# Kernel tuning notes

Measured on AMD Instinct MI355X. Metric: run time of the kernel, lower is better.

Reference implementation:

```python
import jax, jax.numpy as jnp
import numpy as np

SEQ_LEN = 2048
DIM = 1024
HEADS = 16
DIM_HEAD = 64
INNER = HEADS * DIM_HEAD
BASE = 10000.0


def rope_tables(seq_len, head_dim):
    inv_freq = 1.0 / (BASE ** (jnp.arange(0, head_dim, 2, dtype=jnp.float32) / head_dim))
    t = jnp.arange(seq_len, dtype=jnp.float32)
    freqs = jnp.einsum('i,j->ij', t, inv_freq)          # [n, d/2]
    emb = jnp.concatenate([freqs, freqs], axis=-1)       # [n, d]
    return jnp.cos(emb), jnp.sin(emb)                    # each [n, d]


def rotate_half(x):
    d = x.shape[-1] // 2
    return jnp.concatenate([-x[..., d:], x[..., :d]], axis=-1)


def setup_inputs() -> dict:
    key = jax.random.key(0)
    ks = jax.random.split(key, 5)
    x = jax.random.normal(ks[0], (2, SEQ_LEN, DIM), dtype=jnp.float32)
    W_qkv = jax.random.normal(ks[1], (DIM, 3 * INNER), dtype=jnp.float32) * (DIM ** -0.5)
    W_out = jax.random.normal(ks[2], (INNER, DIM), dtype=jnp.float32) * (INNER ** -0.5)
    b_out = jnp.zeros((DIM,), dtype=jnp.float32)
    ln_g = jnp.ones((DIM,), dtype=jnp.float32)
    ln_b = jnp.zeros((DIM,), dtype=jnp.float32)
    return {"x": x, "W_qkv": W_qkv, "W_out": W_out, "b_out": b_out, "ln_g": ln_g, "ln_b": ln_b}


def reference(x, W_qkv, W_out, b_out, ln_g, ln_b):
    b, n, _ = x.shape
    # LayerNorm
    mu = jnp.mean(x, axis=-1, keepdims=True)
    var = jnp.mean(jnp.square(x - mu), axis=-1, keepdims=True)
    xn = (x - mu) * jax.lax.rsqrt(var + 1e-5) * ln_g + ln_b
    # QKV projection -> [b, h, n, d]
    qkv = xn @ W_qkv                                   # [b, n, 3*inner]
    q, k, v = jnp.split(qkv, 3, axis=-1)
    def to_heads(t):
        return t.reshape(b, n, HEADS, DIM_HEAD).transpose(0, 2, 1, 3)
    q, k, v = to_heads(q), to_heads(k), to_heads(v)
    # RoPE
    cos, sin = rope_tables(n, DIM_HEAD)                # [n, d]
    cos = cos[None, None]                              # [1,1,n,d]
    sin = sin[None, None]
    q = q * cos + rotate_half(q) * sin
    k = k * cos + rotate_half(k) * sin
    # Attention
    scale = DIM_HEAD ** -0.5
    dots = jnp.einsum('bhid,bhjd->bhij', q, k) * scale  # [b,h,n,n]
    causal = jnp.tril(jnp.ones((n, n), dtype=bool))
    dots = jnp.where(causal[None, None], dots, jnp.float32(-jnp.inf))
    attn = jax.nn.softmax(dots, axis=-1)
    out = jnp.einsum('bhij,bhjd->bhid', attn, v)       # [b,h,n,d]
    out = out.transpose(0, 2, 1, 3).reshape(b, n, INNER)
    return out @ W_out + b_out
```

## Files before the change

### kernel.cpp

```cpp
#include <hip/hip_runtime.h>
#include <hip/hip_bf16.h>

#define SEQ    2048
#define DMODEL 1024
#define HEADS  16
#define DHEAD  64
#define BATCH  2
#define TOK    (BATCH * SEQ)
#define NQKV   (3 * DMODEL)
#define QK_SCALE (0.125f * 1.4426950408889634f)

typedef __attribute__((ext_vector_type(8))) short bf16x8;
typedef __attribute__((ext_vector_type(4))) float f32x4;

__device__ __forceinline__ float bf2f(ushort u) {
  union { unsigned int i; float f; } v; v.i = ((unsigned int)u) << 16; return v.f;
}
__device__ __forceinline__ ushort f2bf(float f) {
  union { float f; unsigned int i; } v; v.f = f;
  unsigned int r = (v.i + 0x7fffu + ((v.i >> 16) & 1u)) >> 16;
  return (ushort)r;
}

__device__ __forceinline__ int swz(int row, int byteoff) {
  return row * 128 + (byteoff ^ ((row & 7) << 4));
}
__device__ __forceinline__ int kperm(int s) {
  return (s & 0x20) | ((s & 0x0C) << 1) | ((s & 0x10) >> 2) | (s & 3);
}

#define GLL16(g, l)                                                                     \
  __builtin_amdgcn_global_load_lds((const __attribute__((address_space(1))) void*)(g),  \
                                   (__attribute__((address_space(3))) void*)(l), 16, 0, 0)

__global__ __launch_bounds__(256) void ln_kernel(const float* __restrict__ x,
                                                 const float* __restrict__ g,
                                                 const float* __restrict__ b,
                                                 ushort* __restrict__ xn) {
  int t = blockIdx.x;
  int tid = threadIdx.x;
  const float* row = x + (size_t)t * DMODEL;
  float4 v = *(const float4*)(row + tid * 4);
  float s  = v.x + v.y + v.z + v.w;
  float s2 = v.x * v.x + v.y * v.y + v.z * v.z + v.w * v.w;
#pragma unroll
  for (int m = 32; m >= 1; m >>= 1) {
    s  += __shfl_down(s, m);
    s2 += __shfl_down(s2, m);
  }
  __shared__ float ws[4], ws2[4];
  if ((tid & 63) == 0) { ws[tid >> 6] = s; ws2[tid >> 6] = s2; }
  __syncthreads();
  s  = ws[0] + ws[1] + ws[2] + ws[3];
  s2 = ws2[0] + ws2[1] + ws2[2] + ws2[3];
  float mu  = s * (1.f / DMODEL);
  float var = s2 * (1.f / DMODEL) - mu * mu;
  float rs  = rsqrtf(var + 1e-5f);
  float4 gv = *(const float4*)(g + tid * 4);
  float4 bv = *(const float4*)(b + tid * 4);
  ushort4 o;
  o.x = f2bf((v.x - mu) * rs * gv.x + bv.x);
  o.y = f2bf((v.y - mu) * rs * gv.y + bv.y);
  o.z = f2bf((v.z - mu) * rs * gv.z + bv.z);
  o.w = f2bf((v.w - mu) * rs * gv.w + bv.w);
  *(ushort4*)(xn + (size_t)t * DMODEL + tid * 4) = o;
}

__global__ void transpose_f2b(const float* __restrict__ in, ushort* __restrict__ out,
                              int R, int C) {
  __shared__ float tile[32][33];
  int c0 = blockIdx.x * 32, r0 = blockIdx.y * 32;
  int x = threadIdx.x, y = threadIdx.y;
#pragma unroll
  for (int i = 0; i < 32; i += 8) tile[y + i][x] = in[(size_t)(r0 + y + i) * C + c0 + x];
  __syncthreads();
#pragma unroll
  for (int i = 0; i < 32; i += 8) out[(size_t)(c0 + y + i) * R + r0 + x] = f2bf(tile[x][y + i]);
}

__global__ void rope_tab_kernel(float* __restrict__ ct, float* __restrict__ st) {
  int n = blockIdx.x, d = threadIdx.x;
  float invf = expf(-logf(10000.f) * (float)(d & 31) * (1.f / 32.f));
  float a = (float)n * invf;
  ct[n * DHEAD + d] = cosf(a);
  st[n * DHEAD + d] = sinf(a);
}

template<int EPI>
__global__ __launch_bounds__(256) void gemm_bt(const ushort* __restrict__ A,
                                               const ushort* __restrict__ BT,
                                               float* __restrict__ Cf,
                                               const float* __restrict__ bias,
                                               ushort* __restrict__ qh,
                                               ushort* __restrict__ kh,
                                               ushort* __restrict__ vh,
                                               const float* __restrict__ ct,
                                               const float* __restrict__ st,
                                               int M, int N, int K) {
  __shared__ __align__(16) ushort As[128 * 32];
  __shared__ __align__(16) ushort Bs[128 * 32];
  int tid = threadIdx.x;
  int w = tid >> 6, lane = tid & 63;
  int lrow = lane & 15, g = lane >> 4;
  int m0 = blockIdx.y * 128, n0 = blockIdx.x * 128;
  int wr = (w >> 1) * 64, wc = (w & 1) * 64;
  int grow = lane >> 2;
  int gcol = ((lane & 3) ^ ((grow >> 1) & 3)) * 8;
  ushort* ldsA0 = As + w * 512;
  ushort* ldsA1 = As + 2048 + w * 512;
  ushort* ldsB0 = Bs + w * 512;
  ushort* ldsB1 = Bs + 2048 + w * 512;
  int fcol = (g ^ ((lrow >> 1) & 3)) * 8;
  f32x4 acc[4][4] = {};
  for (int k0 = 0; k0 < K; k0 += 32) {
    __syncthreads();
    GLL16(A  + (size_t)(m0 + w * 16 + grow) * K + k0 + gcol, ldsA0);
    GLL16(A  + (size_t)(m0 + 64 + w * 16 + grow) * K + k0 + gcol, ldsA1);
    GLL16(BT + (size_t)(n0 + w * 16 + grow) * K + k0 + gcol, ldsB0);
    GLL16(BT + (size_t)(n0 + 64 + w * 16 + grow) * K + k0 + gcol, ldsB1);
    __syncthreads();
    bf16x8 af[4], bfr[4];
#pragma unroll
    for (int i = 0; i < 4; i++) af[i]  = *(const bf16x8*)(As + (wr + i * 16 + lrow) * 32 + fcol);
#pragma unroll
    for (int i = 0; i < 4; i++) bfr[i] = *(const bf16x8*)(Bs + (wc + i * 16 + lrow) * 32 + fcol);
    __builtin_amdgcn_s_setprio(1);
#pragma unroll
    for (int mf = 0; mf < 4; mf++)
#pragma unroll
      for (int nf = 0; nf < 4; nf++)
        acc[mf][nf] = __builtin_amdgcn_mfma_f32_16x16x32_bf16(af[mf], bfr[nf], acc[mf][nf], 0, 0, 0);
    __builtin_amdgcn_s_setprio(0);
  }
#pragma unroll
  for (int mf = 0; mf < 4; mf++)
#pragma unroll
    for (int nf = 0; nf < 4; nf++) {
      int col = n0 + wc + nf * 16 + lrow;
#pragma unroll
      for (int r = 0; r < 4; r++) {
        int rowi = m0 + wr + mf * 16 + g * 4 + r;
        float val = acc[mf][nf][r];
        if (EPI == 2) {
          Cf[(size_t)rowi * N + col] = val + bias[col];
        } else {
          int mat = col >> 10, c1 = col & 1023;
          int h = c1 >> 6, d = c1 & 63;
          int bb = rowi >> 11, n = rowi & (SEQ - 1);
          if (mat < 2) {
            float partner = acc[mf][nf ^ 2][r];
            float cs = ct[n * DHEAD + d], sn = st[n * DHEAD + d];
            float sgn = (d & 32) ? 1.f : -1.f;
            val = val * cs + sgn * partner * sn;
            if (mat == 0) val *= QK_SCALE;
          }
          ushort* dst = (mat == 0) ? qh : (mat == 1) ? kh : vh;
          dst[((size_t)(bb * HEADS + h) * SEQ + n) * DHEAD + d] = f2bf(val);
        }
      }
    }
}

__global__ __launch_bounds__(256) void attn_kernel(const ushort* __restrict__ q,
                                                   const ushort* __restrict__ k,
                                                   const ushort* __restrict__ v,
                                                   ushort* __restrict__ ao) {
  int wgid = blockIdx.x + gridDim.x * blockIdx.y;
  int xcd = wgid & 7, idx = wgid >> 3;
  int bh = xcd * 4 + (idx & 3);
  int qt = 31 - (idx >> 2);
  int tid = threadIdx.x, w = tid >> 6, lane = tid & 63;
  int lrow = lane & 15, g = lane >> 4;
  __shared__ __align__(16) ushort Ks[2][64 * 64];
  __shared__ __align__(16) ushort Vt[2][64 * 64];
  const ushort* qb = q + (size_t)bh * SEQ * DHEAD;
  const ushort* kb = k + (size_t)bh * SEQ * DHEAD;
  const ushort* vb = v + (size_t)bh * SEQ * DHEAD;
  const ushort* qp = qb + (size_t)(qt * 64 + w * 16 + lrow) * DHEAD + g * 8;
  bf16x8 qf0 = *(const bf16x8*)(qp), qf1 = *(const bf16x8*)(qp + 32);
  f32x4 aO[4] = {};
  float l_s = 0.f;

  int krow = tid >> 2, kco = (tid & 3) * 16;
  int pik = kperm(krow);
  int d0 = (tid & 31) * 2, kv8 = (tid >> 5) * 8;
  int4 ka0, ka1;
  unsigned int vd[8];

#define STAGE_ISSUE(j)                                                          \
  {                                                                             \
    const ushort* ks = kb + ((size_t)((j) * 64 + pik)) * DHEAD + kco;           \
    ka0 = *(const int4*)ks;                                                     \
    ka1 = *(const int4*)(ks + 8);                                               \
    const ushort* vs = vb + ((size_t)((j) * 64 + kv8)) * DHEAD + d0;            \
    _Pragma("unroll")                                                           \
    for (int jj = 0; jj < 8; jj++) vd[jj] = *(const unsigned int*)(vs + jj * DHEAD); \
  }

#define STAGE_WRITE(bsel)                                                       \
  {                                                                             \
    char* kd = (char*)Ks[bsel];                                                 \
    *(int4*)(kd + swz(krow, (tid & 3) * 32)) = ka0;                             \
    *(int4*)(kd + swz(krow, (tid & 3) * 32 + 16)) = ka1;                        \
    unsigned int lo[4], hi[4];                                                  \
    _Pragma("unroll")                                                           \
    for (int jj = 0; jj < 4; jj++) {                                            \
      lo[jj] = __builtin_amdgcn_perm(vd[2 * jj + 1], vd[2 * jj], 0x05040100u);  \
      hi[jj] = __builtin_amdgcn_perm(vd[2 * jj + 1], vd[2 * jj], 0x07060302u);  \
    }                                                                           \
    char* vdst = (char*)Vt[bsel];                                               \
    *(int4*)(vdst + swz(d0, kv8 * 2))     = *(int4*)lo;                         \
    *(int4*)(vdst + swz(d0 + 1, kv8 * 2)) = *(int4*)hi;                         \
  }

  STAGE_ISSUE(0);
  STAGE_WRITE(0);
  __syncthreads();
  int cur = 0;

  for (int jt = 0; jt <= qt; jt++) {
    if (jt < qt) STAGE_ISSUE(jt + 1);
    const char* kbuf = (const char*)Ks[cur];
    const char* vbuf = (const char*)Vt[cur];
    bf16x8 kf[8];
#pragma unroll
    for (int nf = 0; nf < 4; nf++) {
      kf[2 * nf]     = *(const bf16x8*)(kbuf + swz(nf * 16 + lrow, g * 16));
      kf[2 * nf + 1] = *(const bf16x8*)(kbuf + swz(nf * 16 + lrow, g * 16 + 64));
    }
    bf16x8 pa0, pa1;
    {
      f32x4 aS[4] = {};
      __builtin_amdgcn_s_setprio(1);
#pragma unroll
      for (int nf = 0; nf < 4; nf++) {
        aS[nf] = __builtin_amdgcn_mfma_f32_16x16x32_bf16(kf[2 * nf], qf0, aS[nf], 0, 0, 0);
        aS[nf] = __builtin_amdgcn_mfma_f32_16x16x32_bf16(kf[2 * nf + 1], qf1, aS[nf], 0, 0, 0);
      }
      __builtin_amdgcn_s_setprio(0);
      union { bf16x8 v; __hip_bfloat162 h[4]; } a0, a1;
      bool diag = (jt == qt);
#pragma unroll
      for (int nf = 0; nf < 4; nf++) {
        float p[4];
#pragma unroll
        for (int r = 0; r < 4; r++) {
          int kvl = (nf >> 1) * 32 + g * 8 + (nf & 1) * 4 + r;
          p[r] = exp2f(aS[nf][r]);
          if (diag && kvl > w * 16 + lrow) p[r] = 0.f;
          l_s += p[r];
        }
        __hip_bfloat162 plo = __float22bfloat162_rn({p[0], p[1]});
        __hip_bfloat162 phi = __float22bfloat162_rn({p[2], p[3]});
        if (nf < 2) { a0.h[(nf & 1) * 2] = plo; a0.h[(nf & 1) * 2 + 1] = phi; }
        else        { a1.h[(nf & 1) * 2] = plo; a1.h[(nf & 1) * 2 + 1] = phi; }
      }
      pa0 = a0.v; pa1 = a1.v;
    }
    bf16x8 vf[8];
#pragma unroll
    for (int nf = 0; nf < 4; nf++) {
      vf[2 * nf]     = *(const bf16x8*)(vbuf + swz(nf * 16 + lrow, g * 16));
      vf[2 * nf + 1] = *(const bf16x8*)(vbuf + swz(nf * 16 + lrow, g * 16 + 64));
    }
    __builtin_amdgcn_s_setprio(1);
#pragma unroll
    for (int nf = 0; nf < 4; nf++) {
      aO[nf] = __builtin_amdgcn_mfma_f32_16x16x32_bf16(pa0, vf[2 * nf], aO[nf], 0, 0, 0);
      aO[nf] = __builtin_amdgcn_mfma_f32_16x16x32_bf16(pa1, vf[2 * nf + 1], aO[nf], 0, 0, 0);
    }
    __builtin_amdgcn_s_setprio(0);
    if (jt < qt) STAGE_WRITE(cur ^ 1);
    __syncthreads();
    cur ^= 1;
  }

  l_s += __shfl_xor(l_s, 16);
  l_s += __shfl_xor(l_s, 32);
  int b = bh >> 4, h = bh & 15;
#pragma unroll
  for (int r = 0; r < 4; r++) {
    float inv = 1.f / __shfl(l_s, g * 4 + r);
#pragma unroll
    for (int nf = 0; nf < 4; nf++) {
      int col = h * DHEAD + nf * 16 + lrow;
      int tok = b * SEQ + qt * 64 + w * 16 + g * 4 + r;
      ao[(size_t)tok * DMODEL + col] = f2bf(aO[nf][r] * inv);
    }
  }
#undef STAGE_ISSUE
#undef STAGE_WRITE
}

extern "C" void kernel_launch(void* const* d_in, const int* in_sizes, int n_in,
                              void* d_out, int out_size, void* d_ws, size_t ws_size,
                              hipStream_t stream) {
  const float* x    = (const float*)d_in[0];
  const float* Wqkv = (const float*)d_in[1];
  const float* Wout = (const float*)d_in[2];
  const float* bout = (const float*)d_in[3];
  const float* lng  = (const float*)d_in[4];
  const float* lnb  = (const float*)d_in[5];
  float* out = (float*)d_out;

  ushort* xn    = (ushort*)d_ws;
  ushort* WqkvT = xn + (size_t)TOK * DMODEL;
  ushort* WoutT = WqkvT + (size_t)NQKV * DMODEL;
  ushort* qh    = WoutT + (size_t)DMODEL * DMODEL;
  ushort* kh    = qh + (size_t)BATCH * HEADS * SEQ * DHEAD;
  ushort* vh    = kh + (size_t)BATCH * HEADS * SEQ * DHEAD;
  float*  ct    = (float*)(vh + (size_t)BATCH * HEADS * SEQ * DHEAD);
  float*  st    = ct + SEQ * DHEAD;
  ushort* ao    = xn;

  hipLaunchKernelGGL(ln_kernel, dim3(TOK), dim3(256), 0, stream, x, lng, lnb, xn);
  hipLaunchKernelGGL(transpose_f2b, dim3(NQKV / 32, DMODEL / 32), dim3(32, 8), 0, stream,
                     Wqkv, WqkvT, DMODEL, NQKV);
  hipLaunchKernelGGL(transpose_f2b, dim3(DMODEL / 32, DMODEL / 32), dim3(32, 8), 0, stream,
                     Wout, WoutT, DMODEL, DMODEL);
  hipLaunchKernelGGL(rope_tab_kernel, dim3(SEQ), dim3(DHEAD), 0, stream, ct, st);
  hipLaunchKernelGGL(gemm_bt<1>, dim3(NQKV / 128, TOK / 128), dim3(256), 0, stream,
                     xn, WqkvT, (float*)nullptr, (const float*)nullptr,
                     qh, kh, vh, ct, st, TOK, NQKV, DMODEL);
  hipLaunchKernelGGL(attn_kernel, dim3(32, 32), dim3(256), 0, stream,
                     qh, kh, vh, ao);
  hipLaunchKernelGGL(gemm_bt<2>, dim3(DMODEL / 128, TOK / 128), dim3(256), 0, stream,
                     ao, WoutT, out, bout,
                     (ushort*)nullptr, (ushort*)nullptr, (ushort*)nullptr,
                     (const float*)nullptr, (const float*)nullptr, TOK, DMODEL, DMODEL);
}
```

Before: 131.8 us.

## Replace QKV GEMM with 256x256-tile 8-wave pipelined kernel

Adds a dedicated QKV projection kernel that uses 256x256 output tiles, 512 threads, BK=64 and 128KB of dynamic LDS. It double-buffers A and prefetches B two k-steps ahead with XOR-swizzled LDS and explicit waitcnt/barrier scheduling. This is meant to raise MFMA utilisation and data reuse per tile. The trade-off is a 192-block grid on a 256-CU device and single-block occupancy because of the LDS footprint. The output GEMM becomes its own non-templated kernel with only the bias epilogue.

```diff
diff --git a/kernel.cpp b/kernel.cpp
--- a/kernel.cpp
+++ b/kernel.cpp
@@ -86,17 +86,128 @@
   st[n * DHEAD + d] = sinf(a);
 }
 
-template<int EPI>
-__global__ __launch_bounds__(256) void gemm_bt(const ushort* __restrict__ A,
-                                               const ushort* __restrict__ BT,
-                                               float* __restrict__ Cf,
-                                               const float* __restrict__ bias,
-                                               ushort* __restrict__ qh,
-                                               ushort* __restrict__ kh,
-                                               ushort* __restrict__ vh,
-                                               const float* __restrict__ ct,
-                                               const float* __restrict__ st,
-                                               int M, int N, int K) {
+__global__ __launch_bounds__(512, 2) void gemm_qkv_8p(const ushort* __restrict__ A,
+                                                      const ushort* __restrict__ BT,
+                                                      ushort* __restrict__ qh,
+                                                      ushort* __restrict__ kh,
+                                                      ushort* __restrict__ vh,
+                                                      const float* __restrict__ ct,
+                                                      const float* __restrict__ st,
+                                                      int M, int N, int K) {
+  extern __shared__ ushort smem[];
+  int tid = threadIdx.x;
+  int wid = tid >> 6, lane = tid & 63;
+  int wm = wid >> 2, wn = wid & 3;
+  int lrow = lane & 15, g = lane >> 4;
+  int m0 = blockIdx.y * 256, n0 = blockIdx.x * 256;
+  int rr = tid >> 3, sl = tid & 7;
+  int ss = sl ^ (rr & 7);
+  int nk = K >> 6;
+  f32x4 acc[8][4] = {};
+
+#define STA8(dst, kt, h, j)                                                         \
+  GLL16(A + (size_t)(m0 + (h) * 128 + (j) * 64 + rr) * K + (kt) * 64 + ss * 8,      \
+        (dst) + ((h) * 128 + (j) * 64 + rr) * 64 + sl * 8)
+#define STB8(dst, kt, h, j)                                                         \
+  GLL16(BT + (size_t)(n0 + (h) * 128 + (j) * 64 + rr) * K + (kt) * 64 + ss * 8,     \
+        (dst) + ((h) * 128 + (j) * 64 + rr) * 64 + sl * 8)
+#define BARR() asm volatile("s_barrier" ::: "memory")
+
+  {
+    ushort* b0 = smem + 32768;
+    ushort* b1 = smem + 49152;
+    ushort* a0 = smem;
+    STB8(b0, 0, 0, 0); STB8(b0, 0, 0, 1); STB8(b0, 0, 1, 0); STB8(b0, 0, 1, 1);
+    STA8(a0, 0, 0, 0); STA8(a0, 0, 0, 1); STA8(a0, 0, 1, 0); STA8(a0, 0, 1, 1);
+    STB8(b1, 1, 0, 0); STB8(b1, 1, 0, 1); STB8(b1, 1, 1, 0); STB8(b1, 1, 1, 1);
+  }
+  asm volatile("s_waitcnt vmcnt(4)" ::: "memory");
+  BARR();
+  __builtin_amdgcn_sched_barrier(0);
+
+  for (int kt = 0; kt < nk; ++kt) {
+    const ushort* Ar = smem + ((kt & 1) << 14);
+    ushort* Asn = smem + (((kt + 1) & 1) << 14);
+    ushort* Br  = smem + 32768 + ((kt & 1) << 14);
+    bf16x8 brf[4][2];
+#pragma unroll
+    for (int q = 0; q < 4; ++q) {
+      if (q == 0)      { if (kt + 1 < nk) { STA8(Asn, kt + 1, 0, 0); STA8(Asn, kt + 1, 0, 1); } }
+      else if (q == 1) { if (kt + 1 < nk) { STA8(Asn, kt + 1, 1, 0); STA8(Asn, kt + 1, 1, 1); } }
+      else if (q == 2) { if (kt + 2 < nk) { STB8(Br, kt + 2, 0, 0); STB8(Br, kt + 2, 0, 1); } }
+      else             { if (kt + 2 < nk) { STB8(Br, kt + 2, 1, 0); STB8(Br, kt + 2, 1, 1); } }
+      if (q == 0) {
+#pragma unroll
+        for (int nf = 0; nf < 4; ++nf)
+#pragma unroll
+          for (int ks = 0; ks < 2; ++ks) {
+            int r = wn * 64 + nf * 16 + lrow;
+            brf[nf][ks] = *(const bf16x8*)((const char*)Br + r * 128 +
+                                           ((ks * 64 + g * 16) ^ ((r & 7) << 4)));
+          }
+      }
+      bf16x8 arf[2][2];
+#pragma unroll
+      for (int i = 0; i < 2; ++i)
+#pragma unroll
+        for (int ks = 0; ks < 2; ++ks) {
+          int r = wm * 128 + (2 * q + i) * 16 + lrow;
+          arf[i][ks] = *(const bf16x8*)((const char*)Ar + r * 128 +
+                                        ((ks * 64 + g * 16) ^ ((r & 7) << 4)));
+        }
+      asm volatile("s_waitcnt lgkmcnt(0)" ::: "memory");
+      __builtin_amdgcn_sched_barrier(0);
+      __builtin_amdgcn_s_setprio(1);
+#pragma unroll
+      for (int ks = 0; ks < 2; ++ks)
+#pragma unroll
+        for (int i = 0; i < 2; ++i)
+#pragma unroll
+          for (int nf = 0; nf < 4; ++nf)
+            acc[2 * q + i][nf] = __builtin_amdgcn_mfma_f32_16x16x32_bf16(
+                arf[i][ks], brf[nf][ks], acc[2 * q + i][nf], 0, 0, 0);
+      __builtin_amdgcn_s_setprio(0);
+      if (q < 3) BARR();
+    }
+    if (kt + 2 < nk) asm volatile("s_waitcnt vmcnt(4)" ::: "memory");
+    else             asm volatile("s_waitcnt vmcnt(0)" ::: "memory");
+    BARR();
+    __builtin_amdgcn_sched_barrier(0);
+  }
+#undef STA8
+#undef STB8
+#undef BARR
+
+#pragma unroll
+  for (int mf = 0; mf < 8; ++mf)
+#pragma unroll
+    for (int nf = 0; nf < 4; ++nf) {
+      int col = n0 + wn * 64 + nf * 16 + lrow;
+      int mat = col >> 10, c1 = col & 1023;
+      int h = c1 >> 6, d = c1 & 63;
+#pragma unroll
+      for (int r = 0; r < 4; ++r) {
+        int rowi = m0 + wm * 128 + mf * 16 + g * 4 + r;
+        int bb = rowi >> 11, n = rowi & (SEQ - 1);
+        float val = acc[mf][nf][r];
+        if (mat < 2) {
+          float partner = acc[mf][nf ^ 2][r];
+          float cs = ct[n * DHEAD + d], sn = st[n * DHEAD + d];
+          float sgn = (d & 32) ? 1.f : -1.f;
+          val = val * cs + sgn * partner * sn;
+          if (mat == 0) val *= QK_SCALE;
+        }
+        ushort* dst = (mat == 0) ? qh : (mat == 1) ? kh : vh;
+        dst[((size_t)(bb * HEADS + h) * SEQ + n) * DHEAD + d] = f2bf(val);
+      }
+    }
+}
+
+__global__ __launch_bounds__(256) void gemm_out(const ushort* __restrict__ A,
+                                                const ushort* __restrict__ BT,
+                                                float* __restrict__ Cf,
+                                                const float* __restrict__ bias,
+                                                int M, int N, int K) {
   __shared__ __align__(16) ushort As[128 * 32];
   __shared__ __align__(16) ushort Bs[128 * 32];
   int tid = threadIdx.x;
@@ -140,23 +251,7 @@
 #pragma unroll
       for (int r = 0; r < 4; r++) {
         int rowi = m0 + wr + mf * 16 + g * 4 + r;
-        float val = acc[mf][nf][r];
-        if (EPI == 2) {
-          Cf[(size_t)rowi * N + col] = val + bias[col];
-        } else {
-          int mat = col >> 10, c1 = col & 1023;
-          int h = c1 >> 6, d = c1 & 63;
-          int bb = rowi >> 11, n = rowi & (SEQ - 1);
-          if (mat < 2) {
-            float partner = acc[mf][nf ^ 2][r];
-            float cs = ct[n * DHEAD + d], sn = st[n * DHEAD + d];
-            float sgn = (d & 32) ? 1.f : -1.f;
-            val = val * cs + sgn * partner * sn;
-            if (mat == 0) val *= QK_SCALE;
-          }
-          ushort* dst = (mat == 0) ? qh : (mat == 1) ? kh : vh;
-          dst[((size_t)(bb * HEADS + h) * SEQ + n) * DHEAD + d] = f2bf(val);
-        }
+        Cf[(size_t)rowi * N + col] = acc[mf][nf][r] + bias[col];
       }
     }
 }
@@ -319,13 +414,10 @@
   hipLaunchKernelGGL(transpose_f2b, dim3(DMODEL / 32, DMODEL / 32), dim3(32, 8), 0, stream,
                      Wout, WoutT, DMODEL, DMODEL);
   hipLaunchKernelGGL(rope_tab_kernel, dim3(SEQ), dim3(DHEAD), 0, stream, ct, st);
-  hipLaunchKernelGGL(gemm_bt<1>, dim3(NQKV / 128, TOK / 128), dim3(256), 0, stream,
-                     xn, WqkvT, (float*)nullptr, (const float*)nullptr,
-                     qh, kh, vh, ct, st, TOK, NQKV, DMODEL);
+  hipLaunchKernelGGL(gemm_qkv_8p, dim3(NQKV / 256, TOK / 256), dim3(512), 131072, stream,
+                     xn, WqkvT, qh, kh, vh, ct, st, TOK, NQKV, DMODEL);
   hipLaunchKernelGGL(attn_kernel, dim3(32, 32), dim3(256), 0, stream,
                      qh, kh, vh, ao);
-  hipLaunchKernelGGL(gemm_bt<2>, dim3(DMODEL / 128, TOK / 128), dim3(256), 0, stream,
-                     ao, WoutT, out, bout,
-                     (ushort*)nullptr, (ushort*)nullptr, (ushort*)nullptr,
-                     (const float*)nullptr, (const float*)nullptr, TOK, DMODEL, DMODEL);
-}
+  hipLaunchKernelGGL(gemm_out, dim3(DMODEL / 128, TOK / 128), dim3(256), 0, stream,
+                     ao, WoutT, out, bout, TOK, DMODEL, DMODEL);
+}
```

Result: slower. 144.9 us (+9.9%).
